# Optimization experiments

Measured on AMD Instinct MI355X. Metric: run time of the kernel, lower is better.

The kernel has to match this reference:

```python
import jax, jax.numpy as jnp
import numpy as np

N = 50000

def _norm_coeffs(edge_index, n):
    # add self-loops, compute symmetric GCN normalization D^-1/2 (A+I) D^-1/2
    loops = jnp.arange(n, dtype=edge_index.dtype)
    src = jnp.concatenate([edge_index[0], loops])
    dst = jnp.concatenate([edge_index[1], loops])
    deg = jax.ops.segment_sum(jnp.ones_like(dst, dtype=jnp.float32), dst, num_segments=n)
    dinv = jnp.where(deg > 0, jax.lax.rsqrt(deg), 0.0)
    norm = dinv[src] * dinv[dst]  # [E+N]
    return src, dst, norm

def _gcn(x, W, b, src, dst, norm, n):
    h = x @ W                                   # [N, out]
    m = h[src] * norm[:, None]                  # [E+N, out] gather + scale
    return jax.ops.segment_sum(m, dst, num_segments=n) + b

def setup_inputs() -> dict:
    key = jax.random.key(0)
    ks = jax.random.split(key, 8)
    d, h = 96, 96
    E = 800000
    return {
        "x": jax.random.normal(ks[0], (N, d), jnp.float32),
        "edge_index": jax.random.randint(ks[1], (2, E), 0, N, dtype=jnp.int64),
        "h_prev": jax.random.normal(ks[2], (N, h), jnp.float32),
        "Wx": jax.random.normal(ks[3], (d, h), jnp.float32) * (1.0 / np.sqrt(d)),
        "bx": jnp.zeros((h,), jnp.float32),
        "Wuh": jax.random.normal(ks[4], (2 * h, h), jnp.float32) * (1.0 / np.sqrt(2 * h)),
        "buh": jnp.zeros((h,), jnp.float32),
        "Wch": jax.random.normal(ks[5], (2 * h, h), jnp.float32) * (1.0 / np.sqrt(2 * h)),
        "bch": jnp.zeros((h,), jnp.float32),
    }

def reference(x, edge_index, h_prev, Wx, bx, Wuh, buh, Wch, bch):
    n = x.shape[0]
    src, dst, norm = _norm_coeffs(edge_index, n)
    x_gcn = _gcn(x, Wx, bx, src, dst, norm, n)
    combined = jnp.concatenate([x_gcn, h_prev], axis=1)
    # original computes gcn_uh(combined) twice for u and r; identical math -> compute once
    g = jax.nn.sigmoid(_gcn(combined, Wuh, buh, src, dst, norm, n))
    u = g
    r = g
    combined_r = jnp.concatenate([x_gcn, r * h_prev], axis=1)
    c = jnp.tanh(_gcn(combined_r, Wch, bch, src, dst, norm, n))
    return u * h_prev + (1.0 - u) * c
```

## Files before the change

kernel.cpp:

```cpp
#include <hip/hip_runtime.h>
#include <hip/hip_bf16.h>

#define D 96
#define CAP 64
typedef long long i64;
typedef unsigned short u16;

typedef __bf16 bf16x8 __attribute__((ext_vector_type(8)));
typedef float f32x4 __attribute__((ext_vector_type(4)));

__device__ __forceinline__ float bf2f(u16 u) {
  union { unsigned u; float f; } x; x.u = ((unsigned)u) << 16; return x.f;
}
__device__ __forceinline__ void unpack8(uint4 p, float* a) {
  a[0] = bf2f((u16)(p.x & 0xffff)); a[1] = bf2f((u16)(p.x >> 16));
  a[2] = bf2f((u16)(p.y & 0xffff)); a[3] = bf2f((u16)(p.y >> 16));
  a[4] = bf2f((u16)(p.z & 0xffff)); a[5] = bf2f((u16)(p.z >> 16));
  a[6] = bf2f((u16)(p.w & 0xffff)); a[7] = bf2f((u16)(p.w >> 16));
}

__device__ __forceinline__ void split8(const float* v8, bf16x8& hi, bf16x8& lo) {
  unsigned hu[4], lu[4];
#pragma unroll
  for (int p = 0; p < 4; p++) {
    float v0 = v8[2 * p], v1 = v8[2 * p + 1];
    unsigned u0 = __float_as_uint(v0), u1 = __float_as_uint(v1);
    hu[p] = (u0 >> 16) | (u1 & 0xffff0000u);
    float l0 = v0 - __uint_as_float(u0 & 0xffff0000u);
    float l1 = v1 - __uint_as_float(u1 & 0xffff0000u);
    lu[p] = (__float_as_uint(l0) >> 16) | (__float_as_uint(l1) & 0xffff0000u);
  }
  union { uint4 q; bf16x8 v; } H, L;
  H.q = make_uint4(hu[0], hu[1], hu[2], hu[3]);
  L.q = make_uint4(lu[0], lu[1], lu[2], lu[3]);
  hi = H.v; lo = L.v;
}

__global__ __launch_bounds__(256) void k_build(
    const int* __restrict__ e32, const i64* __restrict__ e64,
    const unsigned* __restrict__ eiw,
    const float* __restrict__ Wx, const float* __restrict__ Wuh,
    const float* __restrict__ Wch,
    u16* __restrict__ wxh, u16* __restrict__ wxl,
    u16* __restrict__ wuhh, u16* __restrict__ wuhl,
    u16* __restrict__ wchh, u16* __restrict__ wchl,
    uint2* __restrict__ region, int* __restrict__ cntmat,
    int E, int N, int NB) {
  const int tid = threadIdx.x;
  if (blockIdx.x >= 256) {
    int cid = (blockIdx.x - 256) * 256 + tid;
    const float* W; u16 *oh, *ol; int loc;
    if (cid < 1152) { W = Wx; oh = wxh; ol = wxl; loc = cid; }
    else if (cid < 3456) { W = Wuh; oh = wuhh; ol = wuhl; loc = cid - 1152; }
    else if (cid < 5760) { W = Wch; oh = wchh; ol = wchl; loc = cid - 3456; }
    else return;
    int oct = loc / 96;
    int j = loc - oct * 96;
    int k0 = oct * 8;
    unsigned hu[4], lu[4];
#pragma unroll
    for (int p = 0; p < 4; p++) {
      float v0 = W[(size_t)(k0 + 2 * p) * D + j];
      float v1 = W[(size_t)(k0 + 2 * p + 1) * D + j];
      unsigned u0 = __float_as_uint(v0), u1 = __float_as_uint(v1);
      hu[p] = (u0 >> 16) | (u1 & 0xffff0000u);
      float l0 = v0 - __uint_as_float(u0 & 0xffff0000u);
      float l1 = v1 - __uint_as_float(u1 & 0xffff0000u);
      lu[p] = (__float_as_uint(l0) >> 16) | (__float_as_uint(l1) & 0xffff0000u);
    }
    *(uint4*)&oh[(size_t)loc * 8] = make_uint4(hu[0], hu[1], hu[2], hu[3]);
    *(uint4*)&ol[(size_t)loc * 8] = make_uint4(lu[0], lu[1], lu[2], lu[3]);
    return;
  }
  __shared__ unsigned fsh[256];
  __shared__ int lofs[256];
  {
    unsigned a = 0;
    int lim = (E < 2048) ? E : 2048;
    for (int j = tid; j < lim; j += 256) a |= eiw[2 * j + 1];
    fsh[tid] = a;
    __syncthreads();
    if (tid < 128) fsh[tid] |= fsh[tid + 128];
    __syncthreads();
    if (tid < 64) {
      unsigned b = fsh[tid] | fsh[tid + 64];
#pragma unroll
      for (int off = 32; off > 0; off >>= 1) b |= __shfl_down(b, off, 64);
      if (tid == 0) fsh[0] = b;
    }
    __syncthreads();
  }
  const int f = (fsh[0] == 0) ? 1 : 0;
  lofs[tid] = 0;
  __syncthreads();
  const int blk = blockIdx.x;
  const int chunk = (E + 255) / 256;
  const int lo = blk * chunk;
  const int hi = min(E, lo + chunk);
  for (int i = lo + tid; i < hi; i += 256) {
    int d, s;
    if (f) { d = (int)e64[(size_t)E + i]; s = (int)e64[i]; }
    else   { d = e32[(size_t)E + i];      s = e32[i]; }
    if ((unsigned)d >= (unsigned)N || (unsigned)s >= (unsigned)N) continue;
    int q = d >> 8;
    int r = atomicAdd(&lofs[q], 1);
    if (r < CAP)
      region[((size_t)q * 256 + blk) * CAP + r] = make_uint2((unsigned)s, (unsigned)d);
  }
  __syncthreads();
  if (tid < NB) cntmat[blk * 256 + tid] = min(lofs[tid], CAP);
}

__global__ __launch_bounds__(256) void k_csr_g1(
    const uint2* __restrict__ region, const int* __restrict__ cntmat,
    int* __restrict__ deg, int* __restrict__ csrp,
    const float* __restrict__ x,
    const u16* __restrict__ whi, const u16* __restrict__ wlo,
    __hip_bfloat16* __restrict__ t, int NB, int N) {
  __shared__ int ldeg[256];
  __shared__ int lcsr[256 * CAP];
  const int tid = threadIdx.x;
  const int b = blockIdx.x;
  ldeg[tid] = 0;
  __syncthreads();
  int cnt = cntmat[tid * 256 + b];
  const uint2* cell = region + ((size_t)b * 256 + tid) * CAP;
  for (int k = 0; k < cnt; k++) {
    uint2 e = cell[k];
    int node = (int)(e.y & 255u);
    int r = atomicAdd(&ldeg[node], 1);
    if (r < CAP) lcsr[node * CAP + r] = (int)e.x;
  }
  __syncthreads();
  deg[(b << 8) + tid] = ldeg[tid];
  const uint4* src = (const uint4*)lcsr;
  uint4* dst = (uint4*)(csrp + ((size_t)b << 8) * CAP);
#pragma unroll
  for (int it = 0; it < (256 * CAP) / 4 / 256; it++)
    dst[tid + it * 256] = src[tid + it * 256];

  const int l = tid & 63;
  const int wv = tid >> 6;
  const int j16 = l & 15;
  const int koct = l >> 4;
#define COLT1(CT, ACC) do {                                                 \
    union { uint4 q; bf16x8 v; } Bh, Bl;                                    \
    const size_t wb = (so + (CT)*16 + j16) * 8;                             \
    Bh.q = *(const uint4*)&whi[wb];                                         \
    Bl.q = *(const uint4*)&wlo[wb];                                         \
    ACC = __builtin_amdgcn_mfma_f32_16x16x32_bf16(ah, Bh.v, ACC, 0, 0, 0);  \
    ACC = __builtin_amdgcn_mfma_f32_16x16x32_bf16(al, Bh.v, ACC, 0, 0, 0);  \
    ACC = __builtin_amdgcn_mfma_f32_16x16x32_bf16(ah, Bl.v, ACC, 0, 0, 0);  \
  } while (0)
#pragma unroll 1
  for (int tt = 0; tt < 4; tt++) {
    const int rloc = wv * 64 + tt * 16;
    const int row = (b << 8) + rloc + j16;
    const bool rok = row < N;
    f32x4 c0, c1, c2, c3, c4, c5;
#pragma unroll
    for (int i = 0; i < 4; i++) { c0[i] = 0.f; c1[i] = 0.f; c2[i] = 0.f;
                                  c3[i] = 0.f; c4[i] = 0.f; c5[i] = 0.f; }
#pragma unroll
    for (int ss = 0; ss < 3; ss++) {
      const int kb = ss * 32 + koct * 8;
      float a8[8] = {0.f, 0.f, 0.f, 0.f, 0.f, 0.f, 0.f, 0.f};
      if (rok) {
        float4 va = *(const float4*)&x[(size_t)row * D + kb];
        float4 vb = *(const float4*)&x[(size_t)row * D + kb + 4];
        a8[0] = va.x; a8[1] = va.y; a8[2] = va.z; a8[3] = va.w;
        a8[4] = vb.x; a8[5] = vb.y; a8[6] = vb.z; a8[7] = vb.w;
      }
      bf16x8 ah, al;
      split8(a8, ah, al);
      const size_t so = (size_t)(ss * 4 + koct) * 96;
      COLT1(0, c0); COLT1(1, c1); COLT1(2, c2);
      COLT1(3, c3); COLT1(4, c4); COLT1(5, c5);
    }
    const int r0loc = rloc + koct * 4;
#pragma unroll
    for (int r = 0; r < 4; r++) {
      int lr0 = r0loc + r;
      int orow = (b << 8) + lr0;
      if (orow >= N) continue;
      float dvv = rsqrtf((float)ldeg[lr0] + 1.0f);
      __hip_bfloat16* tp = &t[(size_t)orow * D + j16];
      tp[0]  = __float2bfloat16(c0[r] * dvv);
      tp[16] = __float2bfloat16(c1[r] * dvv);
      tp[32] = __float2bfloat16(c2[r] * dvv);
      tp[48] = __float2bfloat16(c3[r] * dvv);
      tp[64] = __float2bfloat16(c4[r] * dvv);
      tp[80] = __float2bfloat16(c5[r] * dvv);
    }
  }
#undef COLT1
}

template <int PHASE>
__global__ __launch_bounds__(192) void k_fuse(
    const __hip_bfloat16* __restrict__ tin, const int* __restrict__ deg,
    const int* __restrict__ csrp, const float* __restrict__ bias,
    const float* __restrict__ xgin, const float* __restrict__ hprev,
    const u16* __restrict__ whi, const u16* __restrict__ wlo,
    float* __restrict__ vout, __hip_bfloat16* __restrict__ tout, int N) {
  __shared__ int lidx[16 * 65];
  __shared__ int ldeg[16];
  __shared__ float vl[16][100];
  __shared__ float lcomb[64][25];
  const int tid = threadIdx.x;
  const int vbase = blockIdx.x * 16;
#pragma unroll
  for (int it = 0; it < 6; it++) {
    int i = tid + it * 192;
    if (i < 1024) {
      int n2 = i >> 6, j2 = i & 63;
      lidx[n2 * 65 + j2] = csrp[((size_t)(vbase + n2)) * CAP + j2];
    }
  }
  if (tid < 16) ldeg[tid] = deg[vbase + tid];
  __syncthreads();
  const int n = tid / 12;
  const int c8 = tid - n * 12;
  const int v = vbase + n;
  const int nb = min(ldeg[n], CAP);
  const uint4* t8 = (const uint4*)tin;
  float acc[8] = {0.f, 0.f, 0.f, 0.f, 0.f, 0.f, 0.f, 0.f};
  if (v < N) unpack8(t8[(size_t)v * 12 + c8], acc);
  const int* ip = &lidx[n * 65];
  int j = 0;
  for (; j + 8 <= nb; j += 8) {
    int s0 = ip[j],     s1 = ip[j + 1], s2 = ip[j + 2], s3 = ip[j + 3];
    int s4 = ip[j + 4], s5 = ip[j + 5], s6 = ip[j + 6], s7 = ip[j + 7];
    uint4 p0 = t8[(size_t)s0 * 12 + c8];
    uint4 p1 = t8[(size_t)s1 * 12 + c8];
    uint4 p2 = t8[(size_t)s2 * 12 + c8];
    uint4 p3 = t8[(size_t)s3 * 12 + c8];
    uint4 p4 = t8[(size_t)s4 * 12 + c8];
    uint4 p5 = t8[(size_t)s5 * 12 + c8];
    uint4 p6 = t8[(size_t)s6 * 12 + c8];
    uint4 p7 = t8[(size_t)s7 * 12 + c8];
    float a0[8], a1[8], a2[8], a3[8], a4[8], a5[8], a6[8], a7[8];
    unpack8(p0, a0); unpack8(p1, a1); unpack8(p2, a2); unpack8(p3, a3);
    unpack8(p4, a4); unpack8(p5, a5); unpack8(p6, a6); unpack8(p7, a7);
#pragma unroll
    for (int q = 0; q < 8; q++)
      acc[q] += ((a0[q] + a1[q]) + (a2[q] + a3[q])) + ((a4[q] + a5[q]) + (a6[q] + a7[q]));
  }
  for (; j + 4 <= nb; j += 4) {
    int s0 = ip[j], s1 = ip[j + 1], s2 = ip[j + 2], s3 = ip[j + 3];
    uint4 p0 = t8[(size_t)s0 * 12 + c8];
    uint4 p1 = t8[(size_t)s1 * 12 + c8];
    uint4 p2 = t8[(size_t)s2 * 12 + c8];
    uint4 p3 = t8[(size_t)s3 * 12 + c8];
    float a0[8], a1[8], a2[8], a3[8];
    unpack8(p0, a0); unpack8(p1, a1); unpack8(p2, a2); unpack8(p3, a3);
#pragma unroll
    for (int q = 0; q < 8; q++) acc[q] += (a0[q] + a1[q]) + (a2[q] + a3[q]);
  }
  for (; j < nb; j++) {
    int s = ip[j];
    float a0[8];
    unpack8(t8[(size_t)s * 12 + c8], a0);
#pragma unroll
    for (int q = 0; q < 8; q++) acc[q] += a0[q];
  }
  {
    float dvv = rsqrtf((float)ldeg[n] + 1.0f);
    float4 bA = ((const float4*)bias)[c8 * 2];
    float4 bB = ((const float4*)bias)[c8 * 2 + 1];
    float z[8] = {dvv * acc[0] + bA.x, dvv * acc[1] + bA.y,
                  dvv * acc[2] + bA.z, dvv * acc[3] + bA.w,
                  dvv * acc[4] + bB.x, dvv * acc[5] + bB.y,
                  dvv * acc[6] + bB.z, dvv * acc[7] + bB.w};
    if (PHASE == 2) {
#pragma unroll
      for (int q = 0; q < 8; q++) z[q] = 1.0f / (1.0f + expf(-z[q]));
    }
#pragma unroll
    for (int q = 0; q < 8; q++) vl[n][c8 * 8 + q] = (v < N) ? z[q] : 0.f;
    if (v < N) {
      const size_t oidx = (size_t)v * 12 + c8;
      ((float4*)vout)[oidx * 2]     = make_float4(z[0], z[1], z[2], z[3]);
      ((float4*)vout)[oidx * 2 + 1] = make_float4(z[4], z[5], z[6], z[7]);
    }
  }
  __syncthreads();
  const int l = tid & 63;
  const int wv = tid >> 6;
  const int j16 = l & 15;
  const int koct = l >> 4;
  const bool act = tid < 128;
  f32x4 c0, c1, c2, c3, c4, c5;
#pragma unroll
  for (int i = 0; i < 4; i++) { c0[i] = 0.f; c1[i] = 0.f; c2[i] = 0.f;
                                c3[i] = 0.f; c4[i] = 0.f; c5[i] = 0.f; }
#define COLT2(CT, ACC) do {                                                 \
    union { uint4 q; bf16x8 v; } Bh, Bl;                                    \
    const size_t wb = (so + (CT)*16 + j16) * 8;                             \
    Bh.q = *(const uint4*)&whi[wb];                                         \
    Bl.q = *(const uint4*)&wlo[wb];                                         \
    ACC = __builtin_amdgcn_mfma_f32_16x16x32_bf16(ah, Bh.v, ACC, 0, 0, 0);  \
    ACC = __builtin_amdgcn_mfma_f32_16x16x32_bf16(al, Bh.v, ACC, 0, 0, 0);  \
    ACC = __builtin_amdgcn_mfma_f32_16x16x32_bf16(ah, Bl.v, ACC, 0, 0, 0);  \
  } while (0)
  if (act) {
    const int row = vbase + j16;
    const bool rok = row < N;
#pragma unroll
    for (int ss = 0; ss < 3; ss++) {
      const int kb = ss * 32 + koct * 8;
      float a8[8] = {0.f, 0.f, 0.f, 0.f, 0.f, 0.f, 0.f, 0.f};
      if (wv == 0) {
        if (PHASE == 1) {
#pragma unroll
          for (int q = 0; q < 8; q++) a8[q] = vl[j16][kb + q];
        } else if (rok) {
          float4 va = *(const float4*)&xgin[(size_t)row * D + kb];
          float4 vb = *(const float4*)&xgin[(size_t)row * D + kb + 4];
          a8[0] = va.x; a8[1] = va.y; a8[2] = va.z; a8[3] = va.w;
          a8[4] = vb.x; a8[5] = vb.y; a8[6] = vb.z; a8[7] = vb.w;
        }
      } else if (rok) {
        float4 va = *(const float4*)&hprev[(size_t)row * D + kb];
        float4 vb = *(const float4*)&hprev[(size_t)row * D + kb + 4];
        a8[0] = va.x; a8[1] = va.y; a8[2] = va.z; a8[3] = va.w;
        a8[4] = vb.x; a8[5] = vb.y; a8[6] = vb.z; a8[7] = vb.w;
        if (PHASE == 2) {
#pragma unroll
          for (int q = 0; q < 8; q++) a8[q] *= vl[j16][kb + q];
        }
      }
      bf16x8 ah, al;
      split8(a8, ah, al);
      const size_t so = (size_t)((wv * 3 + ss) * 4 + koct) * 96;
      COLT2(0, c0); COLT2(1, c1); COLT2(2, c2);
      COLT2(3, c3); COLT2(4, c4); COLT2(5, c5);
    }
  }
#undef COLT2
  if (act && wv == 1) {
#pragma unroll
    for (int r = 0; r < 4; r++) {
      lcomb[l][0 + r]  = c0[r]; lcomb[l][4 + r]  = c1[r];
      lcomb[l][8 + r]  = c2[r]; lcomb[l][12 + r] = c3[r];
      lcomb[l][16 + r] = c4[r]; lcomb[l][20 + r] = c5[r];
    }
  }
  __syncthreads();
  if (!(act && wv == 0)) return;
#pragma unroll
  for (int r = 0; r < 4; r++) {
    c0[r] += lcomb[l][0 + r];  c1[r] += lcomb[l][4 + r];
    c2[r] += lcomb[l][8 + r];  c3[r] += lcomb[l][12 + r];
    c4[r] += lcomb[l][16 + r]; c5[r] += lcomb[l][20 + r];
  }
  const int r0 = koct * 4;
#pragma unroll
  for (int r = 0; r < 4; r++) {
    int orow = vbase + r0 + r;
    if (orow >= N) continue;
    float dvv = rsqrtf((float)ldeg[r0 + r] + 1.0f);
    __hip_bfloat16* tp = &tout[(size_t)orow * D + j16];
    tp[0]  = __float2bfloat16(c0[r] * dvv);
    tp[16] = __float2bfloat16(c1[r] * dvv);
    tp[32] = __float2bfloat16(c2[r] * dvv);
    tp[48] = __float2bfloat16(c3[r] * dvv);
    tp[64] = __float2bfloat16(c4[r] * dvv);
    tp[80] = __float2bfloat16(c5[r] * dvv);
  }
}

__global__ __launch_bounds__(192) void k_gfin(
    const __hip_bfloat16* __restrict__ tin, const int* __restrict__ deg,
    const int* __restrict__ csrp, const float* __restrict__ bias,
    const float* __restrict__ g, const float* __restrict__ hprev,
    float* __restrict__ outf, int N) {
  __shared__ int lidx[16 * 65];
  __shared__ int ldeg[16];
  const int tid = threadIdx.x;
  const int vbase = blockIdx.x * 16;
#pragma unroll
  for (int it = 0; it < 6; it++) {
    int i = tid + it * 192;
    if (i < 1024) {
      int n2 = i >> 6, j2 = i & 63;
      lidx[n2 * 65 + j2] = csrp[((size_t)(vbase + n2)) * CAP + j2];
    }
  }
  if (tid < 16) ldeg[tid] = deg[vbase + tid];
  __syncthreads();
  const int n = tid / 12;
  const int c8 = tid - n * 12;
  const int v = vbase + n;
  if (v >= N) return;
  const uint4* t8 = (const uint4*)tin;
  float acc[8];
  unpack8(t8[(size_t)v * 12 + c8], acc);
  const int nb = min(ldeg[n], CAP);
  const int* ip = &lidx[n * 65];
  int j = 0;
  for (; j + 8 <= nb; j += 8) {
    int s0 = ip[j],     s1 = ip[j + 1], s2 = ip[j + 2], s3 = ip[j + 3];
    int s4 = ip[j + 4], s5 = ip[j + 5], s6 = ip[j + 6], s7 = ip[j + 7];
    uint4 p0 = t8[(size_t)s0 * 12 + c8];
    uint4 p1 = t8[(size_t)s1 * 12 + c8];
    uint4 p2 = t8[(size_t)s2 * 12 + c8];
    uint4 p3 = t8[(size_t)s3 * 12 + c8];
    uint4 p4 = t8[(size_t)s4 * 12 + c8];
    uint4 p5 = t8[(size_t)s5 * 12 + c8];
    uint4 p6 = t8[(size_t)s6 * 12 + c8];
    uint4 p7 = t8[(size_t)s7 * 12 + c8];
    float a0[8], a1[8], a2[8], a3[8], a4[8], a5[8], a6[8], a7[8];
    unpack8(p0, a0); unpack8(p1, a1); unpack8(p2, a2); unpack8(p3, a3);
    unpack8(p4, a4); unpack8(p5, a5); unpack8(p6, a6); unpack8(p7, a7);
#pragma unroll
    for (int q = 0; q < 8; q++)
      acc[q] += ((a0[q] + a1[q]) + (a2[q] + a3[q])) + ((a4[q] + a5[q]) + (a6[q] + a7[q]));
  }
  for (; j + 4 <= nb; j += 4) {
    int s0 = ip[j], s1 = ip[j + 1], s2 = ip[j + 2], s3 = ip[j + 3];
    uint4 p0 = t8[(size_t)s0 * 12 + c8];
    uint4 p1 = t8[(size_t)s1 * 12 + c8];
    uint4 p2 = t8[(size_t)s2 * 12 + c8];
    uint4 p3 = t8[(size_t)s3 * 12 + c8];
    float a0[8], a1[8], a2[8], a3[8];
    unpack8(p0, a0); unpack8(p1, a1); unpack8(p2, a2); unpack8(p3, a3);
#pragma unroll
    for (int q = 0; q < 8; q++) acc[q] += (a0[q] + a1[q]) + (a2[q] + a3[q]);
  }
  for (; j < nb; j++) {
    int s = ip[j];
    float a0[8];
    unpack8(t8[(size_t)s * 12 + c8], a0);
#pragma unroll
    for (int q = 0; q < 8; q++) acc[q] += a0[q];
  }
  float dvv = rsqrtf((float)ldeg[n] + 1.0f);
  float4 bA = ((const float4*)bias)[c8 * 2];
  float4 bB = ((const float4*)bias)[c8 * 2 + 1];
  float z[8] = {dvv * acc[0] + bA.x, dvv * acc[1] + bA.y, dvv * acc[2] + bA.z,
                dvv * acc[3] + bA.w, dvv * acc[4] + bB.x, dvv * acc[5] + bB.y,
                dvv * acc[6] + bB.z, dvv * acc[7] + bB.w};
  const size_t oidx = (size_t)v * 12 + c8;
  float4 uA = ((const float4*)g)[oidx * 2], uB = ((const float4*)g)[oidx * 2 + 1];
  float4 hA = ((const float4*)hprev)[oidx * 2], hB = ((const float4*)hprev)[oidx * 2 + 1];
  float4 oA = make_float4(uA.x * hA.x + (1.0f - uA.x) * tanhf(z[0]),
                          uA.y * hA.y + (1.0f - uA.y) * tanhf(z[1]),
                          uA.z * hA.z + (1.0f - uA.z) * tanhf(z[2]),
                          uA.w * hA.w + (1.0f - uA.w) * tanhf(z[3]));
  float4 oB = make_float4(uB.x * hB.x + (1.0f - uB.x) * tanhf(z[4]),
                          uB.y * hB.y + (1.0f - uB.y) * tanhf(z[5]),
                          uB.z * hB.z + (1.0f - uB.z) * tanhf(z[6]),
                          uB.w * hB.w + (1.0f - uB.w) * tanhf(z[7]));
  ((float4*)outf)[oidx * 2] = oA;
  ((float4*)outf)[oidx * 2 + 1] = oB;
}

extern "C" void kernel_launch(void* const* d_in, const int* in_sizes, int n_in,
                              void* d_out, int out_size, void* d_ws, size_t ws_size,
                              hipStream_t stream) {
  const float* x = (const float*)d_in[0];
  const int* ei32 = (const int*)d_in[1];
  const i64* ei64 = (const i64*)d_in[1];
  const unsigned* eiw = (const unsigned*)d_in[1];
  const float* hp = (const float*)d_in[2];
  const float* Wx = (const float*)d_in[3];
  const float* bx = (const float*)d_in[4];
  const float* Wuh = (const float*)d_in[5];
  const float* buh = (const float*)d_in[6];
  const float* Wch = (const float*)d_in[7];
  const float* bch = (const float*)d_in[8];
  float* out = (float*)d_out;

  const int N = in_sizes[0] / D;
  const int E = in_sizes[1] / 2;
  const size_t NF = (size_t)N * D;
  const int NB = (N + 255) >> 8;
  const int R = NB << 8;

  char* base = (char*)d_ws;
  u16* wxh = (u16*)(base + 256);
  u16* wxl = wxh + 9216;
  u16* wuhh = wxl + 9216;
  u16* wuhl = wuhh + 18432;
  u16* wchh = wuhl + 18432;
  u16* wchl = wchh + 18432;
  int* deg = (int*)(wchl + 18432);
  int* cntmat = deg + R;
  uint2* region = (uint2*)(cntmat + 65536);
  int* csrp = (int*)(region + (size_t)NB * 256 * CAP);
  __hip_bfloat16* tA = (__hip_bfloat16*)(csrp + (size_t)R * CAP);
  __hip_bfloat16* tB = tA + NF;
  float* xg = (float*)(tB + NF);
  float* g = xg + NF;

  const int fb = (N + 15) / 16;

  k_build<<<279, 256, 0, stream>>>(ei32, ei64, eiw, Wx, Wuh, Wch,
                                   wxh, wxl, wuhh, wuhl, wchh, wchl,
                                   region, cntmat, E, N, NB);
  k_csr_g1<<<NB, 256, 0, stream>>>(region, cntmat, deg, csrp, x, wxh, wxl, tA, NB, N);
  k_fuse<1><<<fb, 192, 0, stream>>>(tA, deg, csrp, bx, nullptr, hp,
                                    wuhh, wuhl, xg, tB, N);
  k_fuse<2><<<fb, 192, 0, stream>>>(tB, deg, csrp, buh, xg, hp,
                                    wchh, wchl, g, tA, N);
  k_gfin<<<fb, 192, 0, stream>>>(tA, deg, csrp, bch, g, hp, out, N);
}
```

Before: 263.3 us.

## Process 64 nodes per block and give each MFMA wave a full K reduction

The fused GCN kernels now handle 64 nodes per 768-thread block instead of 16 per 192-thread block. In the dense transform stage, four waves each own a 16-row tile and run the whole 192-wide K loop themselves. This replaces the previous two-wave split-K scheme, which combined partial sums through shared memory and an extra barrier. The aim is to reuse weight loads across more rows per block and drop the cross-wave reduction. In exchange, shared memory per block grows, blocks are larger, and each MFMA wave issues twice as many steps serially.

```diff
diff --git a/kernel.cpp b/kernel.cpp
--- a/kernel.cpp
+++ b/kernel.cpp
@@ -197,27 +197,26 @@
 }
 
 template <int PHASE>
-__global__ __launch_bounds__(192) void k_fuse(
+__global__ __launch_bounds__(768) void k_fuse(
     const __hip_bfloat16* __restrict__ tin, const int* __restrict__ deg,
     const int* __restrict__ csrp, const float* __restrict__ bias,
     const float* __restrict__ xgin, const float* __restrict__ hprev,
     const u16* __restrict__ whi, const u16* __restrict__ wlo,
     float* __restrict__ vout, __hip_bfloat16* __restrict__ tout, int N) {
-  __shared__ int lidx[16 * 65];
-  __shared__ int ldeg[16];
-  __shared__ float vl[16][100];
-  __shared__ float lcomb[64][25];
+  __shared__ int lidx[64 * 65];
+  __shared__ int ldeg[64];
+  __shared__ float vl[64][100];
   const int tid = threadIdx.x;
-  const int vbase = blockIdx.x * 16;
+  const int vbase = blockIdx.x * 64;
 #pragma unroll
   for (int it = 0; it < 6; it++) {
-    int i = tid + it * 192;
-    if (i < 1024) {
+    int i = tid + it * 768;
+    if (i < 4096) {
       int n2 = i >> 6, j2 = i & 63;
       lidx[n2 * 65 + j2] = csrp[((size_t)(vbase + n2)) * CAP + j2];
     }
   }
-  if (tid < 16) ldeg[tid] = deg[vbase + tid];
+  if (tid < 64) ldeg[tid] = deg[vbase + tid];
   __syncthreads();
   const int n = tid / 12;
   const int c8 = tid - n * 12;
@@ -285,11 +284,15 @@
     }
   }
   __syncthreads();
+  const int wavid = tid >> 6;
+  if (wavid >= 4) return;
   const int l = tid & 63;
-  const int wv = tid >> 6;
+  const int tt = wavid;
   const int j16 = l & 15;
   const int koct = l >> 4;
-  const bool act = tid < 128;
+  const int rloc = tt * 16;
+  const int row = vbase + rloc + j16;
+  const bool rok = row < N;
   f32x4 c0, c1, c2, c3, c4, c5;
 #pragma unroll
   for (int i = 0; i < 4; i++) { c0[i] = 0.f; c1[i] = 0.f; c2[i] = 0.f;
@@ -303,63 +306,44 @@
     ACC = __builtin_amdgcn_mfma_f32_16x16x32_bf16(al, Bh.v, ACC, 0, 0, 0);  \
     ACC = __builtin_amdgcn_mfma_f32_16x16x32_bf16(ah, Bl.v, ACC, 0, 0, 0);  \
   } while (0)
-  if (act) {
-    const int row = vbase + j16;
-    const bool rok = row < N;
-#pragma unroll
-    for (int ss = 0; ss < 3; ss++) {
-      const int kb = ss * 32 + koct * 8;
-      float a8[8] = {0.f, 0.f, 0.f, 0.f, 0.f, 0.f, 0.f, 0.f};
-      if (wv == 0) {
-        if (PHASE == 1) {
-#pragma unroll
-          for (int q = 0; q < 8; q++) a8[q] = vl[j16][kb + q];
-        } else if (rok) {
-          float4 va = *(const float4*)&xgin[(size_t)row * D + kb];
-          float4 vb = *(const float4*)&xgin[(size_t)row * D + kb + 4];
-          a8[0] = va.x; a8[1] = va.y; a8[2] = va.z; a8[3] = va.w;
-          a8[4] = vb.x; a8[5] = vb.y; a8[6] = vb.z; a8[7] = vb.w;
-        }
+#pragma unroll
+  for (int s = 0; s < 6; s++) {
+    const int kh = s < 3 ? 0 : 1;
+    const int kb = (s - kh * 3) * 32 + koct * 8;
+    float a8[8] = {0.f, 0.f, 0.f, 0.f, 0.f, 0.f, 0.f, 0.f};
+    if (kh == 0) {
+      if (PHASE == 1) {
+#pragma unroll
+        for (int q = 0; q < 8; q++) a8[q] = vl[rloc + j16][kb + q];
       } else if (rok) {
-        float4 va = *(const float4*)&hprev[(size_t)row * D + kb];
-        float4 vb = *(const float4*)&hprev[(size_t)row * D + kb + 4];
+        float4 va = *(const float4*)&xgin[(size_t)row * D + kb];
+        float4 vb = *(const float4*)&xgin[(size_t)row * D + kb + 4];
         a8[0] = va.x; a8[1] = va.y; a8[2] = va.z; a8[3] = va.w;
         a8[4] = vb.x; a8[5] = vb.y; a8[6] = vb.z; a8[7] = vb.w;
-        if (PHASE == 2) {
-#pragma unroll
-          for (int q = 0; q < 8; q++) a8[q] *= vl[j16][kb + q];
-        }
       }
-      bf16x8 ah, al;
-      split8(a8, ah, al);
-      const size_t so = (size_t)((wv * 3 + ss) * 4 + koct) * 96;
-      COLT2(0, c0); COLT2(1, c1); COLT2(2, c2);
-      COLT2(3, c3); COLT2(4, c4); COLT2(5, c5);
-    }
+    } else if (rok) {
+      float4 va = *(const float4*)&hprev[(size_t)row * D + kb];
+      float4 vb = *(const float4*)&hprev[(size_t)row * D + kb + 4];
+      a8[0] = va.x; a8[1] = va.y; a8[2] = va.z; a8[3] = va.w;
+      a8[4] = vb.x; a8[5] = vb.y; a8[6] = vb.z; a8[7] = vb.w;
+      if (PHASE == 2) {
+#pragma unroll
+        for (int q = 0; q < 8; q++) a8[q] *= vl[rloc + j16][kb + q];
+      }
+    }
+    bf16x8 ah, al;
+    split8(a8, ah, al);
+    const size_t so = (size_t)(s * 4 + koct) * 96;
+    COLT2(0, c0); COLT2(1, c1); COLT2(2, c2);
+    COLT2(3, c3); COLT2(4, c4); COLT2(5, c5);
   }
 #undef COLT2
-  if (act && wv == 1) {
-#pragma unroll
-    for (int r = 0; r < 4; r++) {
-      lcomb[l][0 + r]  = c0[r]; lcomb[l][4 + r]  = c1[r];
-      lcomb[l][8 + r]  = c2[r]; lcomb[l][12 + r] = c3[r];
-      lcomb[l][16 + r] = c4[r]; lcomb[l][20 + r] = c5[r];
-    }
-  }
-  __syncthreads();
-  if (!(act && wv == 0)) return;
+  const int r0loc = rloc + koct * 4;
 #pragma unroll
   for (int r = 0; r < 4; r++) {
-    c0[r] += lcomb[l][0 + r];  c1[r] += lcomb[l][4 + r];
-    c2[r] += lcomb[l][8 + r];  c3[r] += lcomb[l][12 + r];
-    c4[r] += lcomb[l][16 + r]; c5[r] += lcomb[l][20 + r];
-  }
-  const int r0 = koct * 4;
-#pragma unroll
-  for (int r = 0; r < 4; r++) {
-    int orow = vbase + r0 + r;
+    int orow = vbase + r0loc + r;
     if (orow >= N) continue;
-    float dvv = rsqrtf((float)ldeg[r0 + r] + 1.0f);
+    float dvv = rsqrtf((float)ldeg[r0loc + r] + 1.0f);
     __hip_bfloat16* tp = &tout[(size_t)orow * D + j16];
     tp[0]  = __float2bfloat16(c0[r] * dvv);
     tp[16] = __float2bfloat16(c1[r] * dvv);
@@ -370,24 +354,24 @@
   }
 }
 
-__global__ __launch_bounds__(192) void k_gfin(
+__global__ __launch_bounds__(768) void k_gfin(
     const __hip_bfloat16* __restrict__ tin, const int* __restrict__ deg,
     const int* __restrict__ csrp, const float* __restrict__ bias,
     const float* __restrict__ g, const float* __restrict__ hprev,
     float* __restrict__ outf, int N) {
-  __shared__ int lidx[16 * 65];
-  __shared__ int ldeg[16];
+  __shared__ int lidx[64 * 65];
+  __shared__ int ldeg[64];
   const int tid = threadIdx.x;
-  const int vbase = blockIdx.x * 16;
+  const int vbase = blockIdx.x * 64;
 #pragma unroll
   for (int it = 0; it < 6; it++) {
-    int i = tid + it * 192;
-    if (i < 1024) {
+    int i = tid + it * 768;
+    if (i < 4096) {
       int n2 = i >> 6, j2 = i & 63;
       lidx[n2 * 65 + j2] = csrp[((size_t)(vbase + n2)) * CAP + j2];
     }
   }
-  if (tid < 16) ldeg[tid] = deg[vbase + tid];
+  if (tid < 64) ldeg[tid] = deg[vbase + tid];
   __syncthreads();
   const int n = tid / 12;
   const int c8 = tid - n * 12;
@@ -494,15 +478,15 @@
   float* xg = (float*)(tB + NF);
   float* g = xg + NF;
 
-  const int fb = (N + 15) / 16;
+  const int fb64 = (N + 63) / 64;
 
   k_build<<<279, 256, 0, stream>>>(ei32, ei64, eiw, Wx, Wuh, Wch,
                                    wxh, wxl, wuhh, wuhl, wchh, wchl,
                                    region, cntmat, E, N, NB);
   k_csr_g1<<<NB, 256, 0, stream>>>(region, cntmat, deg, csrp, x, wxh, wxl, tA, NB, N);
-  k_fuse<1><<<fb, 192, 0, stream>>>(tA, deg, csrp, bx, nullptr, hp,
-                                    wuhh, wuhl, xg, tB, N);
-  k_fuse<2><<<fb, 192, 0, stream>>>(tB, deg, csrp, buh, xg, hp,
-                                    wchh, wchl, g, tA, N);
-  k_gfin<<<fb, 192, 0, stream>>>(tA, deg, csrp, bch, g, hp, out, N);
-}
+  k_fuse<1><<<fb64, 768, 0, stream>>>(tA, deg, csrp, bx, nullptr, hp,
+                                      wuhh, wuhl, xg, tB, N);
+  k_fuse<2><<<fb64, 768, 0, stream>>>(tB, deg, csrp, buh, xg, hp,
+                                      wchh, wchl, g, tA, N);
+  k_gfin<<<fb64, 768, 0, stream>>>(tA, deg, csrp, bch, g, hp, out, N);
+}
```

After: 259.9 us. Within noise of the previous version (-1.3%).
